# Kernel optimization log

Hardware: AMD Instinct MI355X
Metric: run time of the kernel (lower is better)

The kernel has to match this reference:

```python
import jax, jax.numpy as jnp
import numpy as np

KS = 17  # structuring element size
R = KS // 2  # radius 8


def _ellipse_kernel():
    # replicates cv2.getStructuringElement(cv2.MORPH_ELLIPSE, (17, 17)):
    # per row dy, fill columns within dx = round(sqrt(r^2 - dy^2))
    k = np.zeros((KS, KS), np.float32)
    for i in range(KS):
        dy = i - R
        dx = int(round(np.sqrt(max(0.0, float(R * R - dy * dy)))))
        k[i, R - dx:R + dx + 1] = 1.0
    return k


def _morph(v, kern, erode):
    # exact TF min-plus erosion2d / max-plus dilation2d with SAME padding
    # (pad +inf for erosion, -inf for dilation), filters = kern per channel.
    B, H, W, C = v.shape
    pad_val = np.inf if erode else -np.inf
    sgn = -1.0 if erode else 1.0
    red = jnp.min if erode else jnp.max
    comb = jnp.minimum if erode else jnp.maximum
    vp = jnp.pad(v, ((0, 0), (0, 0), (R, R), (0, 0)), constant_values=pad_val)
    X = jnp.stack([vp[:, :, k:k + W, :] for k in range(KS)], axis=0)
    # per kernel row dy: 1D min/max-plus correlation along x
    rows = [red(X + sgn * kern[dy][:, None, None, None, None], axis=0) for dy in range(KS)]
    Rst = jnp.pad(jnp.stack(rows, axis=0), ((0, 0), (0, 0), (R, R), (0, 0), (0, 0)), constant_values=pad_val)
    out = Rst[0][:, 0:H]
    for dy in range(1, KS):
        out = comb(out, Rst[dy][:, dy:dy + H])
    return out


def _mask_edges(masks, kern):
    # flip border rows/cols (corners flipped twice -> original)
    m = jnp.concatenate([1.0 - masks[:, :1], masks[:, 1:-1], 1.0 - masks[:, -1:]], axis=1)
    m = jnp.concatenate([1.0 - m[:, :, :1], m[:, :, 1:-1], 1.0 - m[:, :, -1:]], axis=2)
    eroded = _morph(m, kern, erode=True) + 1.0
    dilated = _morph(m, kern, erode=False) - 1.0
    return dilated - eroded


def setup_inputs() -> dict:
    key = jax.random.key(0)
    k1, k2, k3 = jax.random.split(key, 3)
    B, H, W, C = 8, 512, 512, 3
    in_detections = jax.random.randint(k1, (B, H, W, C), 0, 2).astype(jnp.float32)
    p_detections = jax.random.normal(k2, (B, H, W, C), dtype=jnp.float32)
    edge_weight = 1.0 + 39.0 * jax.random.uniform(k3, (1, 1, 1, C), dtype=jnp.float32)
    in_masks = jnp.ones((B, C), dtype=jnp.float32)
    logvars = -3.0 * jnp.ones((1, C), dtype=jnp.float32)
    return {"in_masks": in_masks, "in_detections": in_detections,
            "p_detections": p_detections, "edge_weight": edge_weight,
            "logvars": logvars}


def reference(in_masks, in_detections, p_detections, edge_weight, logvars):
    kern = jnp.asarray(_ellipse_kernel())
    edges = _mask_edges(in_detections, kern)  # (B,H,W,C)
    weights = 1.0 + (edge_weight - 1.0) * edges
    weights = weights / jnp.sum(weights, axis=(1, 2), keepdims=True)
    pix = jnp.where(in_detections == 1.0,
                    jnp.maximum(0.0, 1.0 - p_detections) ** 2,
                    jnp.maximum(0.0, p_detections) ** 2)
    raw = jnp.sum(weights * pix, axis=(1, 2))  # (B,C)
    losses = jnp.exp(-logvars) * raw + logvars  # (B,C)
    return jnp.mean(in_masks * losses, axis=1)  # (B,)
```

## Files before the change

kernel.cpp:

```cpp
#include <hip/hip_runtime.h>
#include <stdint.h>


#define TILE 16
#define ROWS 32
#define NT   32
#define PLS  90

__global__ __launch_bounds__(1024) void k_fused(const float* __restrict__ det,
                                                const float* __restrict__ pdet,
                                                float* __restrict__ partials) {
  __shared__ uint64_t mb[3][ROWS][9];
  __shared__ uint64_t pl[ROWS][PLS];
  __shared__ uint64_t eg[3][TILE][8];
  __shared__ float red[16][6];
  __shared__ int cw[3][2];

  int blk = blockIdx.x;
  int b = blk & 7;
  int tile = blk >> 3;
  int r0 = tile * TILE;
  int tid = threadIdx.x;
  int wv = tid >> 6, lane = tid & 63;

  for (int it = 0; it < 16; ++it) {
    int task = wv * 16 + it;
    int rl = task >> 3, w = task & 7;
    int grow = r0 - 8 + rl;
    uint64_t b0 = 0, b1 = 0, b2 = 0;
    if (grow >= 0 && grow < 512) {
      size_t base = (((((size_t)b << 9) + grow) << 9) + (w << 6) + lane) * 3;
      float d0 = det[base], d1 = det[base + 1], d2 = det[base + 2];
      b0 = __ballot(d0 == 1.0f);
      b1 = __ballot(d1 == 1.0f);
      b2 = __ballot(d2 == 1.0f);
    }
    if (lane == 0) { mb[0][rl][w] = b0; mb[1][rl][w] = b1; mb[2][rl][w] = b2; }
  }
  __syncthreads();

  const int PD[9] = {5, 5, 5, 4, 4, 3, 2, 1, 0};

  for (int ch = 0; ch < 3; ++ch) {
    if (tid < 256) {
      int rl = tid >> 3, w = tid & 7;
      int grow = r0 - 8 + rl;
      bool valid = (grow >= 0 && grow < 512);
      uint64_t x = 0, xl = 0, xh = 0;
      if (valid) {
        x = mb[ch][rl][w];
        xl = (w > 0) ? mb[ch][rl][w - 1] : 0;
        xh = (w < 7) ? mb[ch][rl][w + 1] : 0;
        if (grow == 0 || grow == 511) {
          x = ~x;
          xl = (w > 0) ? ~xl : 0;
          xh = (w < 7) ? ~xh : 0;
        }
        if (w == 0) x ^= 1ull;
        if (w == 7) x ^= (1ull << 63);
      }
      uint64_t* P = pl[rl];
      P[0 * 8 + w] = x;
      uint64_t d = x;
#pragma unroll
      for (int s = 1; s <= 8; ++s) {
        d |= (x << s) | (xl >> (64 - s)) | (x >> s) | (xh << (64 - s));
        if (s >= 4) P[(s - 3) * 8 + w] = d;
      }
      uint64_t xc = 0, xlc = 0, xhc = 0;
      if (valid) {
        xc = ~x;
        xlc = (w > 0) ? ~xl : 0;
        xhc = (w < 7) ? ~xh : 0;
      }
      d = xc;
#pragma unroll
      for (int s = 1; s <= 8; ++s) {
        d |= (xc << s) | (xlc >> (64 - s)) | (xc >> s) | (xhc << (64 - s));
        if (s >= 4) P[(s + 2) * 8 + w] = d;
      }
    }
    __syncthreads();

    if (tid < 128) {
      int rl = tid >> 3, w = tid & 7;
      uint64_t dil = 0, erc = 0;
#pragma unroll
      for (int dy = -8; dy <= 8; ++dy) {
        int ady = dy < 0 ? -dy : dy;
        int pr = rl + 8 + dy;
        if (ady == 8) {
          int grow = r0 - 8 + pr;
          uint64_t m = pl[pr][w];
          dil |= m;
          erc |= (grow >= 0 && grow < 512) ? ~m : 0;
        } else {
          dil |= pl[pr][PD[ady] * 8 + w];
          erc |= pl[pr][(PD[ady] + 5) * 8 + w];
        }
      }
      uint64_t e = dil & erc;
      eg[ch][rl][w] = e;
      int c = __popcll(e);
#pragma unroll
      for (int off = 32; off >= 1; off >>= 1) c += __shfl_xor(c, off);
      if (lane == 0) cw[ch][wv] = c;
    }
    __syncthreads();
  }

  float sA0 = 0, sA1 = 0, sA2 = 0, sE0 = 0, sE1 = 0, sE2 = 0;
#pragma unroll
  for (int it = 0; it < 8; ++it) {
    int task = wv * 8 + it;
    int rl = task >> 3, w = task & 7;
    int grow = r0 + rl;
    size_t base = (((((size_t)b << 9) + grow) << 9) + (w << 6) + lane) * 3;
    float p0 = pdet[base], p1 = pdet[base + 1], p2 = pdet[base + 2];
    uint64_t D0 = mb[0][rl + 8][w], D1 = mb[1][rl + 8][w], D2 = mb[2][rl + 8][w];
    uint64_t E0 = eg[0][rl][w], E1 = eg[1][rl][w], E2 = eg[2][rl][w];
    float v0 = ((D0 >> lane) & 1) ? 1.0f - p0 : p0; v0 = fmaxf(v0, 0.f); v0 *= v0;
    float v1 = ((D1 >> lane) & 1) ? 1.0f - p1 : p1; v1 = fmaxf(v1, 0.f); v1 *= v1;
    float v2 = ((D2 >> lane) & 1) ? 1.0f - p2 : p2; v2 = fmaxf(v2, 0.f); v2 *= v2;
    sA0 += v0; sA1 += v1; sA2 += v2;
    if ((E0 >> lane) & 1) sE0 += v0;
    if ((E1 >> lane) & 1) sE1 += v1;
    if ((E2 >> lane) & 1) sE2 += v2;
  }
#pragma unroll
  for (int off = 32; off >= 1; off >>= 1) {
    sA0 += __shfl_xor(sA0, off); sA1 += __shfl_xor(sA1, off); sA2 += __shfl_xor(sA2, off);
    sE0 += __shfl_xor(sE0, off); sE1 += __shfl_xor(sE1, off); sE2 += __shfl_xor(sE2, off);
  }
  if (lane == 0) {
    red[wv][0] = sA0; red[wv][1] = sA1; red[wv][2] = sA2;
    red[wv][3] = sE0; red[wv][4] = sE1; red[wv][5] = sE2;
  }
  __syncthreads();

  if (tid < 6) {
    float s = 0.f;
    for (int i = 0; i < 16; ++i) s += red[i][tid];
    partials[blk * 9 + tid] = s;
  } else if (tid < 9) {
    int ch = tid - 6;
    partials[blk * 9 + tid] = (float)(cw[ch][0] + cw[ch][1]);
  }
}

__global__ __launch_bounds__(64) void k_final(const float* __restrict__ partials,
                                              const float* __restrict__ in_masks,
                                              const float* __restrict__ ew,
                                              const float* __restrict__ lv,
                                              float* __restrict__ out) {
  int b = threadIdx.x;
  if (b >= 8) return;
  float acc = 0.f;
  for (int ch = 0; ch < 3; ++ch) {
    float sA = 0.f, sE = 0.f, cn = 0.f;
    for (int t = 0; t < NT; ++t) {
      const float* P = partials + ((t << 3) | b) * 9;
      sA += P[ch]; sE += P[3 + ch]; cn += P[6 + ch];
    }
    float w1 = ew[ch] - 1.0f;
    float S = 262144.0f + w1 * cn;
    float raw = (sA + w1 * sE) / S;
    float loss = expf(-lv[ch]) * raw + lv[ch];
    acc += in_masks[b * 3 + ch] * loss;
  }
  out[b] = acc * (1.0f / 3.0f);
}

extern "C" void kernel_launch(void* const* d_in, const int* in_sizes, int n_in,
                              void* d_out, int out_size, void* d_ws, size_t ws_size,
                              hipStream_t stream) {
  const float* in_masks = (const float*)d_in[0];
  const float* det = (const float*)d_in[1];
  const float* pdet = (const float*)d_in[2];
  const float* ew = (const float*)d_in[3];
  const float* lv = (const float*)d_in[4];
  float* out = (float*)d_out;

  float* partials = (float*)d_ws;

  k_fused<<<256, 1024, 0, stream>>>(det, pdet, partials);
  k_final<<<1, 64, 0, stream>>>(partials, in_masks, ew, lv, out);
}
```

Baseline: 24.64 us.

## Fuse final reduction via cooperative grid sync and split dilation/erosion passes

Merges the final per-batch reduction kernel into the main kernel with a cooperative launch and a grid-wide sync, removing a second kernel launch. It also spreads the horizontal dilation and complement-dilation bitmask work over 512 threads instead of 256, so each thread does one pass. The trade-off is the cost of a cooperative launch and grid barrier across 256 blocks of 1024 threads. All blocks must be co-resident for the barrier to work, which should hold on a device with enough compute units.

```diff
diff --git a/kernel.cpp b/kernel.cpp
--- a/kernel.cpp
+++ b/kernel.cpp
@@ -1,5 +1,8 @@
 #include <hip/hip_runtime.h>
+#include <hip/hip_cooperative_groups.h>
 #include <stdint.h>
+
+namespace cg = cooperative_groups;
 
 
 #define TILE 16
@@ -7,9 +10,13 @@
 #define NT   32
 #define PLS  90
 
-__global__ __launch_bounds__(1024) void k_fused(const float* __restrict__ det,
-                                                const float* __restrict__ pdet,
-                                                float* __restrict__ partials) {
+__global__ __launch_bounds__(1024) void k_all(const float* __restrict__ det,
+                                              const float* __restrict__ pdet,
+                                              float* __restrict__ partials,
+                                              const float* __restrict__ in_masks,
+                                              const float* __restrict__ ew,
+                                              const float* __restrict__ lv,
+                                              float* __restrict__ out) {
   __shared__ uint64_t mb[3][ROWS][9];
   __shared__ uint64_t pl[ROWS][PLS];
   __shared__ uint64_t eg[3][TILE][8];
@@ -42,8 +49,10 @@
   const int PD[9] = {5, 5, 5, 4, 4, 3, 2, 1, 0};
 
   for (int ch = 0; ch < 3; ++ch) {
-    if (tid < 256) {
-      int rl = tid >> 3, w = tid & 7;
+    if (tid < 512) {
+      int side = tid >> 8;
+      int t2 = tid & 255;
+      int rl = t2 >> 3, w = t2 & 7;
       int grow = r0 - 8 + rl;
       bool valid = (grow >= 0 && grow < 512);
       uint64_t x = 0, xl = 0, xh = 0;
@@ -58,26 +67,19 @@
         }
         if (w == 0) x ^= 1ull;
         if (w == 7) x ^= (1ull << 63);
+        if (side) {
+          x = ~x;
+          xl = (w > 0) ? ~xl : 0;
+          xh = (w < 7) ? ~xh : 0;
+        }
       }
       uint64_t* P = pl[rl];
-      P[0 * 8 + w] = x;
+      if (!side) P[w] = x;
       uint64_t d = x;
 #pragma unroll
       for (int s = 1; s <= 8; ++s) {
         d |= (x << s) | (xl >> (64 - s)) | (x >> s) | (xh << (64 - s));
-        if (s >= 4) P[(s - 3) * 8 + w] = d;
-      }
-      uint64_t xc = 0, xlc = 0, xhc = 0;
-      if (valid) {
-        xc = ~x;
-        xlc = (w > 0) ? ~xl : 0;
-        xhc = (w < 7) ? ~xh : 0;
-      }
-      d = xc;
-#pragma unroll
-      for (int s = 1; s <= 8; ++s) {
-        d |= (xc << s) | (xlc >> (64 - s)) | (xc >> s) | (xhc << (64 - s));
-        if (s >= 4) P[(s + 2) * 8 + w] = d;
+        if (s >= 4) P[(s - 3 + side * 5) * 8 + w] = d;
       }
     }
     __syncthreads();
@@ -143,32 +145,28 @@
     for (int i = 0; i < 16; ++i) s += red[i][tid];
     partials[blk * 9 + tid] = s;
   } else if (tid < 9) {
-    int ch = tid - 6;
-    partials[blk * 9 + tid] = (float)(cw[ch][0] + cw[ch][1]);
+    int chx = tid - 6;
+    partials[blk * 9 + tid] = (float)(cw[chx][0] + cw[chx][1]);
   }
-}
 
-__global__ __launch_bounds__(64) void k_final(const float* __restrict__ partials,
-                                              const float* __restrict__ in_masks,
-                                              const float* __restrict__ ew,
-                                              const float* __restrict__ lv,
-                                              float* __restrict__ out) {
-  int b = threadIdx.x;
-  if (b >= 8) return;
-  float acc = 0.f;
-  for (int ch = 0; ch < 3; ++ch) {
-    float sA = 0.f, sE = 0.f, cn = 0.f;
-    for (int t = 0; t < NT; ++t) {
-      const float* P = partials + ((t << 3) | b) * 9;
-      sA += P[ch]; sE += P[3 + ch]; cn += P[6 + ch];
+  cg::this_grid().sync();
+
+  if (blk == 0 && tid < 8) {
+    int b8 = tid;
+    float acc = 0.f;
+    for (int ch = 0; ch < 3; ++ch) {
+      float sA = 0.f, sE = 0.f, cn = 0.f;
+      for (int t = 0; t < NT; ++t) {
+        const float* P = partials + (size_t)((t << 3) | b8) * 9;
+        sA += P[ch]; sE += P[3 + ch]; cn += P[6 + ch];
+      }
+      float w1 = ew[ch] - 1.0f;
+      float S = 262144.0f + w1 * cn;
+      float raw = (sA + w1 * sE) / S;
+      acc += in_masks[b8 * 3 + ch] * (expf(-lv[ch]) * raw + lv[ch]);
     }
-    float w1 = ew[ch] - 1.0f;
-    float S = 262144.0f + w1 * cn;
-    float raw = (sA + w1 * sE) / S;
-    float loss = expf(-lv[ch]) * raw + lv[ch];
-    acc += in_masks[b * 3 + ch] * loss;
+    out[b8] = acc * (1.0f / 3.0f);
   }
-  out[b] = acc * (1.0f / 3.0f);
 }
 
 extern "C" void kernel_launch(void* const* d_in, const int* in_sizes, int n_in,
@@ -183,6 +181,8 @@
 
   float* partials = (float*)d_ws;
 
-  k_fused<<<256, 1024, 0, stream>>>(det, pdet, partials);
-  k_final<<<1, 64, 0, stream>>>(partials, in_masks, ew, lv, out);
+  void* args[] = {(void*)&det, (void*)&pdet, (void*)&partials,
+                  (void*)&in_masks, (void*)&ew, (void*)&lv, (void*)&out};
+  hipLaunchCooperativeKernel((const void*)k_all, dim3(256), dim3(1024),
+                             args, 0, stream);
 }
```

Measured after the change: 59.54 us. 2.42x slower.

## Decompose ellipse morphology into row-grouped ORs with incremental horizontal dilation

Applied to the files above, without the earlier changes.

Replaces the per-channel two-phase morphology (per-row horizontal dilation planes in shared memory, then a vertical combine, with syncs between them) with a single pass. In that pass 768 threads each OR together rows sharing the same horizontal radius, then grow that radius step by step. The mask and its complement are computed in parallel, and the border flips move into the ballot stage. Edge-pixel counts are gathered in the final reduction, and k_final spreads its work across 24 threads. The aim is fewer barriers, less shared memory, and more threads active in the morphology, at the cost of more redundant row loads per thread.

```diff
diff --git a/kernel.cpp b/kernel.cpp
--- a/kernel.cpp
+++ b/kernel.cpp
@@ -5,16 +5,13 @@
 #define TILE 16
 #define ROWS 32
 #define NT   32
-#define PLS  90
 
 __global__ __launch_bounds__(1024) void k_fused(const float* __restrict__ det,
                                                 const float* __restrict__ pdet,
                                                 float* __restrict__ partials) {
   __shared__ uint64_t mb[3][ROWS][9];
-  __shared__ uint64_t pl[ROWS][PLS];
-  __shared__ uint64_t eg[3][TILE][8];
-  __shared__ float red[16][6];
-  __shared__ int cw[3][2];
+  __shared__ uint64_t dg[2][3][TILE][8];
+  __shared__ float red[16][9];
 
   int blk = blockIdx.x;
   int b = blk & 7;
@@ -34,117 +31,109 @@
       b0 = __ballot(d0 == 1.0f);
       b1 = __ballot(d1 == 1.0f);
       b2 = __ballot(d2 == 1.0f);
+      if (grow == 0 || grow == 511) { b0 = ~b0; b1 = ~b1; b2 = ~b2; }
+      if (w == 0) { b0 ^= 1ull; b1 ^= 1ull; b2 ^= 1ull; }
+      if (w == 7) { b0 ^= 1ull << 63; b1 ^= 1ull << 63; b2 ^= 1ull << 63; }
     }
     if (lane == 0) { mb[0][rl][w] = b0; mb[1][rl][w] = b1; mb[2][rl][w] = b2; }
   }
   __syncthreads();
 
-  const int PD[9] = {5, 5, 5, 4, 4, 3, 2, 1, 0};
+  if (tid < 768) {
+    int side = tid >= 384;
+    int t2 = tid & 383;
+    int ch = t2 >> 7;
+    int rl = (t2 >> 3) & 15;
+    int w = t2 & 7;
 
-  for (int ch = 0; ch < 3; ++ch) {
-    if (tid < 256) {
-      int rl = tid >> 3, w = tid & 7;
-      int grow = r0 - 8 + rl;
-      bool valid = (grow >= 0 && grow < 512);
-      uint64_t x = 0, xl = 0, xh = 0;
-      if (valid) {
-        x = mb[ch][rl][w];
-        xl = (w > 0) ? mb[ch][rl][w - 1] : 0;
-        xh = (w < 7) ? mb[ch][rl][w + 1] : 0;
-        if (grow == 0 || grow == 511) {
-          x = ~x;
-          xl = (w > 0) ? ~xl : 0;
-          xh = (w < 7) ? ~xh : 0;
-        }
-        if (w == 0) x ^= 1ull;
-        if (w == 7) x ^= (1ull << 63);
+    uint64_t V8l = 0, V8m = 0, V8r = 0, V7l = 0, V7m = 0, V7r = 0;
+    uint64_t V6l = 0, V6m = 0, V6r = 0, V5l = 0, V5m = 0, V5r = 0;
+    uint64_t V4l = 0, V4m = 0, V4r = 0, V0m = 0;
+#pragma unroll
+    for (int dy = -8; dy <= 8; ++dy) {
+      int ady = dy < 0 ? -dy : dy;
+      int pr = rl + 8 + dy;
+      uint64_t al = (w > 0) ? mb[ch][pr][w - 1] : 0;
+      uint64_t am = mb[ch][pr][w];
+      uint64_t ar = (w < 7) ? mb[ch][pr][w + 1] : 0;
+      if (side) {
+        int grow = r0 + rl + dy;
+        uint64_t mask = (grow >= 0 && grow < 512) ? ~0ull : 0ull;
+        al = (w > 0) ? (~al & mask) : 0;
+        am = ~am & mask;
+        ar = (w < 7) ? (~ar & mask) : 0;
       }
-      uint64_t* P = pl[rl];
-      P[0 * 8 + w] = x;
-      uint64_t d = x;
+      if (ady <= 2)      { V8l |= al; V8m |= am; V8r |= ar; }
+      else if (ady <= 4) { V7l |= al; V7m |= am; V7r |= ar; }
+      else if (ady == 5) { V6l |= al; V6m |= am; V6r |= ar; }
+      else if (ady == 6) { V5l |= al; V5m |= am; V5r |= ar; }
+      else if (ady == 7) { V4l |= al; V4m |= am; V4r |= ar; }
+      else               { V0m |= am; }
+    }
+    uint64_t l = V8l, m = V8m, r = V8r;
+#define H1STEP() { uint64_t nl = l | (l << 1) | (l >> 1) | (m << 63);           \
+                   uint64_t nm = m | (m << 1) | (l >> 63) | (m >> 1) | (r << 63);\
+                   uint64_t nr = r | (r << 1) | (m >> 63) | (r >> 1);           \
+                   l = nl; m = nm; r = nr; }
+    H1STEP(); l |= V7l; m |= V7m; r |= V7r;
+    H1STEP(); l |= V6l; m |= V6m; r |= V6r;
+    H1STEP(); l |= V5l; m |= V5m; r |= V5r;
+    H1STEP(); l |= V4l; m |= V4m; r |= V4r;
+#undef H1STEP
+    uint64_t outw = m | V0m;
 #pragma unroll
-      for (int s = 1; s <= 8; ++s) {
-        d |= (x << s) | (xl >> (64 - s)) | (x >> s) | (xh << (64 - s));
-        if (s >= 4) P[(s - 3) * 8 + w] = d;
-      }
-      uint64_t xc = 0, xlc = 0, xhc = 0;
-      if (valid) {
-        xc = ~x;
-        xlc = (w > 0) ? ~xl : 0;
-        xhc = (w < 7) ? ~xh : 0;
-      }
-      d = xc;
-#pragma unroll
-      for (int s = 1; s <= 8; ++s) {
-        d |= (xc << s) | (xlc >> (64 - s)) | (xc >> s) | (xhc << (64 - s));
-        if (s >= 4) P[(s + 2) * 8 + w] = d;
-      }
-    }
-    __syncthreads();
-
-    if (tid < 128) {
-      int rl = tid >> 3, w = tid & 7;
-      uint64_t dil = 0, erc = 0;
-#pragma unroll
-      for (int dy = -8; dy <= 8; ++dy) {
-        int ady = dy < 0 ? -dy : dy;
-        int pr = rl + 8 + dy;
-        if (ady == 8) {
-          int grow = r0 - 8 + pr;
-          uint64_t m = pl[pr][w];
-          dil |= m;
-          erc |= (grow >= 0 && grow < 512) ? ~m : 0;
-        } else {
-          dil |= pl[pr][PD[ady] * 8 + w];
-          erc |= pl[pr][(PD[ady] + 5) * 8 + w];
-        }
-      }
-      uint64_t e = dil & erc;
-      eg[ch][rl][w] = e;
-      int c = __popcll(e);
-#pragma unroll
-      for (int off = 32; off >= 1; off >>= 1) c += __shfl_xor(c, off);
-      if (lane == 0) cw[ch][wv] = c;
-    }
-    __syncthreads();
+    for (int s = 1; s <= 4; ++s)
+      outw |= (m << s) | (l >> (64 - s)) | (m >> s) | (r << (64 - s));
+    dg[side][ch][rl][w] = outw;
   }
+  __syncthreads();
 
   float sA0 = 0, sA1 = 0, sA2 = 0, sE0 = 0, sE1 = 0, sE2 = 0;
+  int c0 = 0, c1 = 0, c2 = 0;
 #pragma unroll
   for (int it = 0; it < 8; ++it) {
     int task = wv * 8 + it;
     int rl = task >> 3, w = task & 7;
     int grow = r0 + rl;
-    size_t base = (((((size_t)b << 9) + grow) << 9) + (w << 6) + lane) * 3;
+    int j = (w << 6) + lane;
+    size_t base = (((((size_t)b << 9) + grow) << 9) + j) * 3;
     float p0 = pdet[base], p1 = pdet[base + 1], p2 = pdet[base + 2];
-    uint64_t D0 = mb[0][rl + 8][w], D1 = mb[1][rl + 8][w], D2 = mb[2][rl + 8][w];
-    uint64_t E0 = eg[0][rl][w], E1 = eg[1][rl][w], E2 = eg[2][rl][w];
-    float v0 = ((D0 >> lane) & 1) ? 1.0f - p0 : p0; v0 = fmaxf(v0, 0.f); v0 *= v0;
-    float v1 = ((D1 >> lane) & 1) ? 1.0f - p1 : p1; v1 = fmaxf(v1, 0.f); v1 *= v1;
-    float v2 = ((D2 >> lane) & 1) ? 1.0f - p2 : p2; v2 = fmaxf(v2, 0.f); v2 *= v2;
+    int flip = (int)(grow == 0 || grow == 511) ^ (int)(j == 0 || j == 511);
+    uint64_t M0 = mb[0][rl + 8][w], M1 = mb[1][rl + 8][w], M2 = mb[2][rl + 8][w];
+    uint64_t E0 = dg[0][0][rl][w] & dg[1][0][rl][w];
+    uint64_t E1 = dg[0][1][rl][w] & dg[1][1][rl][w];
+    uint64_t E2 = dg[0][2][rl][w] & dg[1][2][rl][w];
+    int d0 = ((int)(M0 >> lane) & 1) ^ flip;
+    int d1 = ((int)(M1 >> lane) & 1) ^ flip;
+    int d2 = ((int)(M2 >> lane) & 1) ^ flip;
+    float v0 = d0 ? 1.0f - p0 : p0; v0 = fmaxf(v0, 0.f); v0 *= v0;
+    float v1 = d1 ? 1.0f - p1 : p1; v1 = fmaxf(v1, 0.f); v1 *= v1;
+    float v2 = d2 ? 1.0f - p2 : p2; v2 = fmaxf(v2, 0.f); v2 *= v2;
+    int e0 = (int)(E0 >> lane) & 1, e1 = (int)(E1 >> lane) & 1,
+        e2 = (int)(E2 >> lane) & 1;
     sA0 += v0; sA1 += v1; sA2 += v2;
-    if ((E0 >> lane) & 1) sE0 += v0;
-    if ((E1 >> lane) & 1) sE1 += v1;
-    if ((E2 >> lane) & 1) sE2 += v2;
+    c0 += e0; c1 += e1; c2 += e2;
+    if (e0) sE0 += v0;
+    if (e1) sE1 += v1;
+    if (e2) sE2 += v2;
   }
 #pragma unroll
   for (int off = 32; off >= 1; off >>= 1) {
     sA0 += __shfl_xor(sA0, off); sA1 += __shfl_xor(sA1, off); sA2 += __shfl_xor(sA2, off);
     sE0 += __shfl_xor(sE0, off); sE1 += __shfl_xor(sE1, off); sE2 += __shfl_xor(sE2, off);
+    c0 += __shfl_xor(c0, off); c1 += __shfl_xor(c1, off); c2 += __shfl_xor(c2, off);
   }
   if (lane == 0) {
     red[wv][0] = sA0; red[wv][1] = sA1; red[wv][2] = sA2;
     red[wv][3] = sE0; red[wv][4] = sE1; red[wv][5] = sE2;
+    red[wv][6] = (float)c0; red[wv][7] = (float)c1; red[wv][8] = (float)c2;
   }
   __syncthreads();
 
-  if (tid < 6) {
+  if (tid < 9) {
     float s = 0.f;
     for (int i = 0; i < 16; ++i) s += red[i][tid];
     partials[blk * 9 + tid] = s;
-  } else if (tid < 9) {
-    int ch = tid - 6;
-    partials[blk * 9 + tid] = (float)(cw[ch][0] + cw[ch][1]);
   }
 }
 
@@ -153,22 +142,22 @@
                                               const float* __restrict__ ew,
                                               const float* __restrict__ lv,
                                               float* __restrict__ out) {
-  int b = threadIdx.x;
-  if (b >= 8) return;
-  float acc = 0.f;
-  for (int ch = 0; ch < 3; ++ch) {
-    float sA = 0.f, sE = 0.f, cn = 0.f;
-    for (int t = 0; t < NT; ++t) {
-      const float* P = partials + ((t << 3) | b) * 9;
-      sA += P[ch]; sE += P[3 + ch]; cn += P[6 + ch];
-    }
-    float w1 = ew[ch] - 1.0f;
-    float S = 262144.0f + w1 * cn;
-    float raw = (sA + w1 * sE) / S;
-    float loss = expf(-lv[ch]) * raw + lv[ch];
-    acc += in_masks[b * 3 + ch] * loss;
+  int t = threadIdx.x;
+  if (t >= 24) return;
+  int b8 = t / 3, ch = t - 3 * b8;
+  float sA = 0.f, sE = 0.f, cn = 0.f;
+  for (int tl = 0; tl < NT; ++tl) {
+    const float* P = partials + (size_t)((tl << 3) | b8) * 9;
+    sA += P[ch]; sE += P[3 + ch]; cn += P[6 + ch];
   }
-  out[b] = acc * (1.0f / 3.0f);
+  float w1 = ew[ch] - 1.0f;
+  float S = 262144.0f + w1 * cn;
+  float raw = (sA + w1 * sE) / S;
+  float term = in_masks[b8 * 3 + ch] * (expf(-lv[ch]) * raw + lv[ch]);
+  float t0 = __shfl(term, b8 * 3 + 0);
+  float t1 = __shfl(term, b8 * 3 + 1);
+  float t2 = __shfl(term, b8 * 3 + 2);
+  if (ch == 0) out[b8] = (t0 + t1 + t2) * (1.0f / 3.0f);
 }
 
 extern "C" void kernel_launch(void* const* d_in, const int* in_sizes, int n_in,
```

After: 35.02 us. 1.42x slower.
